# Performance work log

Hardware: AMD Instinct MI355X
Metric: run time of the kernel (lower is better)

The kernel has to match this reference:

```python
import jax, jax.numpy as jnp
import numpy as np

N_NODES = 50000
N_EDGES = 800000
IN_CH = 64
HID_CH = 128
LAT_CH = 64
N_GRAPHS = 64
U_DIM = 32


def setup_inputs() -> dict:
    key = jax.random.key(0)
    ks = jax.random.split(key, 12)
    x = jax.random.normal(ks[0], (N_NODES, IN_CH), dtype=jnp.float32)
    edge_index = jax.random.randint(ks[1], (2, N_EDGES), 0, N_NODES, dtype=jnp.int64)
    edge_attr = jax.random.normal(ks[2], (N_EDGES, 8), dtype=jnp.float32)  # unused by NodeModel
    u = jax.random.normal(ks[3], (N_GRAPHS, U_DIM), dtype=jnp.float32)
    batch = jnp.sort(jax.random.randint(ks[4], (N_NODES,), 0, N_GRAPHS, dtype=jnp.int64))
    s = 0.02
    W1 = jax.random.normal(ks[5], (2 * IN_CH, HID_CH), dtype=jnp.float32) * s
    b1 = jnp.zeros((HID_CH,), dtype=jnp.float32)
    W2 = jax.random.normal(ks[6], (HID_CH, HID_CH), dtype=jnp.float32) * s
    b2 = jnp.zeros((HID_CH,), dtype=jnp.float32)
    W3 = jax.random.normal(ks[7], (HID_CH, LAT_CH), dtype=jnp.float32) * s
    b3 = jnp.zeros((LAT_CH,), dtype=jnp.float32)
    return {"x": x, "edge_index": edge_index, "edge_attr": edge_attr, "u": u,
            "batch": batch, "W1": W1, "b1": b1, "W2": W2, "b2": b2, "W3": W3, "b3": b3}


def reference(x, edge_index, edge_attr, u, batch, W1, b1, W2, b2, W3, b3):
    row, col = edge_index[0], edge_index[1]
    # gather endpoints -> [E, 2*in_ch]
    h = jnp.concatenate([x[row], x[col]], axis=1)
    # 3-layer MLP on edges
    h = jax.nn.relu(h @ W1 + b1)
    h = jax.nn.relu(h @ W2 + b2)
    h = h @ W3 + b3  # [E, latent]
    # scatter reductions over destination node (col)
    cnt = jax.ops.segment_sum(jnp.ones((h.shape[0],), h.dtype), col, num_segments=N_NODES)
    mean = jax.ops.segment_sum(h, col, num_segments=N_NODES) / jnp.maximum(cnt, 1.0)[:, None]
    mx = jax.ops.segment_max(h, col, num_segments=N_NODES)
    mn = jax.ops.segment_min(h, col, num_segments=N_NODES)
    nonempty = (cnt > 0)[:, None]
    mx = jnp.where(nonempty, mx, 0.0)  # torch_scatter returns 0 for empty segments
    mn = jnp.where(nonempty, mn, 0.0)
    return jnp.concatenate([x, mean, mx, mn, u[batch]], axis=1)
```

## Files before the change

kernel.cpp:

```cpp
#include <hip/hip_runtime.h>

#define E_EDGES 800000
#define NN 50000
#define OUT_STRIDE 288

typedef __bf16 bf16;
typedef bf16 bf16x8 __attribute__((ext_vector_type(8)));
typedef float floatx4 __attribute__((ext_vector_type(4)));
typedef unsigned short ushort8v __attribute__((ext_vector_type(8)));

__device__ __forceinline__ unsigned short f2bf(float f){
    unsigned u = __float_as_uint(f);
    u += 0x7fffu + ((u >> 16) & 1u);
    return (unsigned short)(u >> 16);
}
__device__ __forceinline__ unsigned pack2bf(float a, float b){
    return (unsigned)f2bf(a) | ((unsigned)f2bf(b) << 16);
}
__device__ __forceinline__ unsigned encf(float f){
    unsigned u = __float_as_uint(f);
    return (u & 0x80000000u) ? ~u : (u | 0x80000000u);
}
__device__ __forceinline__ float decf(unsigned u){
    return __uint_as_float((u & 0x80000000u) ? (u ^ 0x80000000u) : ~u);
}
__device__ __forceinline__ floatx4 mfma16(ushort8v a, ushort8v b, floatx4 c){
    return __builtin_amdgcn_mfma_f32_16x16x32_bf16(
        __builtin_bit_cast(bf16x8, a), __builtin_bit_cast(bf16x8, b), c, 0, 0, 0);
}
__device__ __forceinline__ void flush_run(float* out, int node, float s, float mx, float mn, int lane){
    float* sp = out + (long)node * OUT_STRIDE + 64;
    atomicAdd(sp + lane, s);
    atomicMax((unsigned*)sp + 64 + lane, encf(mx));
    atomicMin((unsigned*)sp + 128 + lane, encf(mn));
}

#define ZC_N   12500
#define INIT_N 2400000
#define XBF_N  800000
#define PK_N   40960
#define SETUP_TOTAL (ZC_N + INIT_N + XBF_N + PK_N)

__global__ void setup_kernel(const float* __restrict__ x,
                             const float* __restrict__ W1, const float* __restrict__ W2,
                             const float* __restrict__ W3,
                             unsigned short* __restrict__ wp, unsigned short* __restrict__ xbf,
                             int* __restrict__ cnt, float* __restrict__ out)
{
    int i = blockIdx.x * blockDim.x + threadIdx.x;
    if (i < ZC_N) {
        ((int4*)cnt)[i] = make_int4(0, 0, 0, 0);
        return;
    }
    i -= ZC_N;
    if (i < INIT_N) {
        int row = i / 48, q = i % 48;
        uint4 val = (q < 32) ? make_uint4(0u, 0u, 0u, 0u)
                             : make_uint4(~0u, ~0u, ~0u, ~0u);
        ((uint4*)out)[(long)row * 72 + 16 + q] = val;
        return;
    }
    i -= INIT_N;
    if (i < XBF_N) {
        float4 v = ((const float4*)x)[i];
        ushort4 o; o.x = f2bf(v.x); o.y = f2bf(v.y); o.z = f2bf(v.z); o.w = f2bf(v.w);
        ((ushort4*)xbf)[i] = o;
        return;
    }
    i -= XBF_N;
    if (i < PK_N) {
        const float* W; int N; int idx;
        if (i < 16384)      { W = W1; N = 128; idx = i; }
        else if (i < 32768) { W = W2; N = 128; idx = i - 16384; }
        else                { W = W3; N = 64;  idx = i - 32768; }
        int j = idx & 7, lane = (idx >> 3) & 63, kc = (idx >> 9) & 3, nt = idx >> 11;
        wp[i] = f2bf(W[(kc * 32 + ((lane >> 4) & 3) * 8 + j) * N + nt * 16 + (lane & 15)]);
    }
}

__global__ void hist_kernel(const int* __restrict__ ei, int* __restrict__ cnt){
    int e = blockIdx.x * blockDim.x + threadIdx.x;
    if (e < E_EDGES) atomicAdd(&cnt[ei[E_EDGES + e]], 1);
}

__global__ void scanA_kernel(const int* __restrict__ cnt, int* __restrict__ off,
                             int* __restrict__ bsum){
    __shared__ int s[256];
    int tid = threadIdx.x;
    int node = blockIdx.x * 196 + tid;
    int val = (tid < 196 && node < NN) ? cnt[node] : 0;
    s[tid] = val;
    __syncthreads();
    for (int d = 1; d < 256; d <<= 1){
        int t = (tid >= d) ? s[tid - d] : 0;
        __syncthreads();
        s[tid] += t;
        __syncthreads();
    }
    if (tid < 196 && node < NN) off[node] = s[tid] - val;
    if (tid == 255) bsum[blockIdx.x] = s[255];
}

__global__ void scanB_kernel(const int* __restrict__ bsum, int* __restrict__ bbase){
    __shared__ int s[256];
    int tid = threadIdx.x;
    int val = bsum[tid];
    s[tid] = val;
    __syncthreads();
    for (int d = 1; d < 256; d <<= 1){
        int t = (tid >= d) ? s[tid - d] : 0;
        __syncthreads();
        s[tid] += t;
        __syncthreads();
    }
    bbase[tid] = s[tid] - val;
}

__global__ void scanC_kernel(int* __restrict__ off, const int* __restrict__ bbase){
    int n = blockIdx.x * blockDim.x + threadIdx.x;
    if (n < NN) off[n] += bbase[n / 196];
}

__global__ void scatter_kernel(const int* __restrict__ ei, int* __restrict__ off,
                               int2* __restrict__ enodes){
    int e = blockIdx.x * blockDim.x + threadIdx.x;
    if (e >= E_EDGES) return;
    int c = ei[E_EDGES + e], r = ei[e];
    int pos = atomicAdd(&off[c], 1);
    enodes[pos] = make_int2(r, c);
}

__global__ __launch_bounds__(256, 4) void edge_mlp_kernel(
    const unsigned short* __restrict__ xbf, const int2* __restrict__ enodes,
    const unsigned short* __restrict__ wp,
    const float* __restrict__ b1, const float* __restrict__ b2, const float* __restrict__ b3,
    float* __restrict__ out)
{
    __shared__ __align__(16) unsigned char smem[4 * 8704];

    const int tid  = threadIdx.x;
    const int lane = tid & 63;
    const int w    = tid >> 6;
    const int quad = lane >> 4;
    const int ln   = lane & 15;
    unsigned short* wbuf = (unsigned short*)(smem + w * 8704);
    float* Tf = (float*)wbuf;
    const ushort8v* wpv = (const ushort8v*)wp;

    const int g = blockIdx.x * 4 + w;
    const int ebase = g * 32;
    int2 ed0 = enodes[ebase + ln];
    int2 ed1 = enodes[ebase + 16 + ln];

    const ushort8v* r0 = (const ushort8v*)(xbf + (long)ed0.x * 64);
    const ushort8v* c0 = (const ushort8v*)(xbf + (long)ed0.y * 64);
    const ushort8v* r1 = (const ushort8v*)(xbf + (long)ed1.x * 64);
    const ushort8v* c1 = (const ushort8v*)(xbf + (long)ed1.y * 64);
    ushort8v B0[4] = { r0[quad], r0[4 + quad], c0[quad], c0[4 + quad] };
    ushort8v B1[4] = { r1[quad], r1[4 + quad], c1[quad], c1[4 + quad] };

#pragma unroll
    for (int nt = 0; nt < 8; nt++){
        floatx4 bini = *(const floatx4*)(b1 + nt * 16 + quad * 4);
        floatx4 a0 = bini, a1 = bini;
#pragma unroll
        for (int kc = 0; kc < 4; kc++){
            ushort8v Af = wpv[(nt * 4 + kc) * 64 + lane];
            a0 = mfma16(Af, B0[kc], a0);
            a1 = mfma16(Af, B1[kc], a1);
        }
        uint2 p0, p1;
        p0.x = pack2bf(fmaxf(a0[0], 0.f), fmaxf(a0[1], 0.f));
        p0.y = pack2bf(fmaxf(a0[2], 0.f), fmaxf(a0[3], 0.f));
        p1.x = pack2bf(fmaxf(a1[0], 0.f), fmaxf(a1[1], 0.f));
        p1.y = pack2bf(fmaxf(a1[2], 0.f), fmaxf(a1[3], 0.f));
        int col = nt * 16 + quad * 4;
        *(uint2*)(wbuf + ln * 136 + col)        = p0;
        *(uint2*)(wbuf + (16 + ln) * 136 + col) = p1;
    }

    ushort8v H0[4], H1[4];
#pragma unroll
    for (int kc = 0; kc < 4; kc++){
        H0[kc] = *(const ushort8v*)(wbuf + ln * 136 + kc * 32 + quad * 8);
        H1[kc] = *(const ushort8v*)(wbuf + (16 + ln) * 136 + kc * 32 + quad * 8);
    }
#pragma unroll
    for (int nt = 0; nt < 8; nt++){
        floatx4 bini = *(const floatx4*)(b2 + nt * 16 + quad * 4);
        floatx4 a0 = bini, a1 = bini;
#pragma unroll
        for (int kc = 0; kc < 4; kc++){
            ushort8v Af = wpv[2048 + (nt * 4 + kc) * 64 + lane];
            a0 = mfma16(Af, H0[kc], a0);
            a1 = mfma16(Af, H1[kc], a1);
        }
        uint2 p0, p1;
        p0.x = pack2bf(fmaxf(a0[0], 0.f), fmaxf(a0[1], 0.f));
        p0.y = pack2bf(fmaxf(a0[2], 0.f), fmaxf(a0[3], 0.f));
        p1.x = pack2bf(fmaxf(a1[0], 0.f), fmaxf(a1[1], 0.f));
        p1.y = pack2bf(fmaxf(a1[2], 0.f), fmaxf(a1[3], 0.f));
        int col = nt * 16 + quad * 4;
        *(uint2*)(wbuf + ln * 136 + col)        = p0;
        *(uint2*)(wbuf + (16 + ln) * 136 + col) = p1;
    }

    ushort8v G0[4], G1[4];
#pragma unroll
    for (int kc = 0; kc < 4; kc++){
        G0[kc] = *(const ushort8v*)(wbuf + ln * 136 + kc * 32 + quad * 8);
        G1[kc] = *(const ushort8v*)(wbuf + (16 + ln) * 136 + kc * 32 + quad * 8);
    }
#pragma unroll
    for (int nt = 0; nt < 4; nt++){
        floatx4 bini = *(const floatx4*)(b3 + nt * 16 + quad * 4);
        floatx4 a0 = bini, a1 = bini;
#pragma unroll
        for (int kc = 0; kc < 4; kc++){
            ushort8v Af = wpv[4096 + (nt * 4 + kc) * 64 + lane];
            a0 = mfma16(Af, G0[kc], a0);
            a1 = mfma16(Af, G1[kc], a1);
        }
        int och = nt * 16 + quad * 4;
#pragma unroll
        for (int r = 0; r < 4; r++){
            Tf[(och + r) * 33 + ln]      = a0[r];
            Tf[(och + r) * 33 + 16 + ln] = a1[r];
        }
    }

    float v[32];
#pragma unroll
    for (int j = 0; j < 32; j++) v[j] = Tf[lane * 33 + j];
    int cn0 = ed0.y, cn1 = ed1.y;
    int cur = __builtin_amdgcn_readlane(cn0, 0);
    float s = v[0], mx = v[0], mn = v[0];
#pragma unroll
    for (int j = 1; j < 32; j++){
        int nj = (j < 16) ? __builtin_amdgcn_readlane(cn0, j)
                          : __builtin_amdgcn_readlane(cn1, j - 16);
        if (nj != cur){
            flush_run(out, cur, s, mx, mn, lane);
            cur = nj; s = v[j]; mx = v[j]; mn = v[j];
        } else {
            s += v[j]; mx = fmaxf(mx, v[j]); mn = fminf(mn, v[j]);
        }
    }
    flush_run(out, cur, s, mx, mn, lane);
}

__global__ void finalize_kernel(const float* __restrict__ x, const float* __restrict__ u,
                                const int* __restrict__ batch, const int* __restrict__ cnt,
                                float* __restrict__ out)
{
    long i = (long)blockIdx.x * blockDim.x + threadIdx.x;
    if (i >= (long)NN * 72) return;
    int ndx = (int)(i / 72);
    int q   = (int)(i % 72);
    float4 res;
    if (q < 16) {
        res = ((const float4*)(x + (long)ndx * 64))[q];
    } else if (q < 32) {
        float4 sv = ((const float4*)out)[i];
        int k = cnt[ndx];
        float inv = 1.f / (float)(k > 0 ? k : 1);
        res.x = sv.x * inv; res.y = sv.y * inv; res.z = sv.z * inv; res.w = sv.w * inv;
    } else if (q < 64) {
        uint4 e = ((const uint4*)out)[i];
        bool ne = cnt[ndx] > 0;
        res.x = ne ? decf(e.x) : 0.f; res.y = ne ? decf(e.y) : 0.f;
        res.z = ne ? decf(e.z) : 0.f; res.w = ne ? decf(e.w) : 0.f;
    } else {
        res = ((const float4*)(u + (long)batch[ndx] * 32))[q - 64];
    }
    ((float4*)out)[i] = res;
}

extern "C" void kernel_launch(void* const* d_in, const int* in_sizes, int n_in,
                              void* d_out, int out_size, void* d_ws, size_t ws_size,
                              hipStream_t stream)
{
    const float* x     = (const float*)d_in[0];
    const int*   ei    = (const int*)d_in[1];
    const float* u     = (const float*)d_in[3];
    const int*   batch = (const int*)d_in[4];
    const float* W1    = (const float*)d_in[5];
    const float* b1    = (const float*)d_in[6];
    const float* W2    = (const float*)d_in[7];
    const float* b2    = (const float*)d_in[8];
    const float* W3    = (const float*)d_in[9];
    const float* b3    = (const float*)d_in[10];
    float* out = (float*)d_out;
    unsigned char* ws = (unsigned char*)d_ws;

    unsigned short* wp     = (unsigned short*)ws;
    int*            cnt    = (int*)(ws + 81920);
    int*            off    = (int*)(ws + 281920);
    int*            bsum   = (int*)(ws + 481920);
    int*            bbase  = (int*)(ws + 482944);
    int2*           enodes = (int2*)(ws + 483968);
    unsigned short* xbf    = (unsigned short*)(ws + 6883968);

    setup_kernel<<<(SETUP_TOTAL + 255) / 256, 256, 0, stream>>>(x, W1, W2, W3, wp, xbf, cnt, out);
    hist_kernel<<<(E_EDGES + 255) / 256, 256, 0, stream>>>(ei, cnt);
    scanA_kernel<<<256, 256, 0, stream>>>(cnt, off, bsum);
    scanB_kernel<<<1, 256, 0, stream>>>(bsum, bbase);
    scanC_kernel<<<(NN + 255) / 256, 256, 0, stream>>>(off, bbase);
    scatter_kernel<<<(E_EDGES + 255) / 256, 256, 0, stream>>>(ei, off, enodes);
    edge_mlp_kernel<<<6250, 256, 0, stream>>>(xbf, enodes, wp, b1, b2, b3, out);
    finalize_kernel<<<(int)(((long)NN * 72 + 255) / 256), 256, 0, stream>>>(x, u, batch, cnt, out);
}
```

Before: 327.7 us.

## Fuse histogram into setup, drop scanC, prefetch weights in MLP kernel

The histogram pass is folded into the setup kernel and the count buffer is zeroed with an async memset instead. The scanC pass is removed by adding the block base inside the scatter kernel. The edge MLP kernel now prefetches weight fragments two tiles ahead into a 3-slot register ring to hide global load latency behind the MFMAs. The bf16 conversion is switched to the compiler's native cast. The prefetch ring raises register pressure and may reduce occupancy, and the merged setup kernel runs atomics alongside streaming writes.

```diff
diff --git a/kernel.cpp b/kernel.cpp
--- a/kernel.cpp
+++ b/kernel.cpp
@@ -10,12 +10,12 @@
 typedef unsigned short ushort8v __attribute__((ext_vector_type(8)));
 
 __device__ __forceinline__ unsigned short f2bf(float f){
-    unsigned u = __float_as_uint(f);
-    u += 0x7fffu + ((u >> 16) & 1u);
-    return (unsigned short)(u >> 16);
+    return __builtin_bit_cast(unsigned short, (bf16)f);
 }
 __device__ __forceinline__ unsigned pack2bf(float a, float b){
-    return (unsigned)f2bf(a) | ((unsigned)f2bf(b) << 16);
+    unsigned short lo = __builtin_bit_cast(unsigned short, (bf16)a);
+    unsigned short hi = __builtin_bit_cast(unsigned short, (bf16)b);
+    return (unsigned)lo | ((unsigned)hi << 16);
 }
 __device__ __forceinline__ unsigned encf(float f){
     unsigned u = __float_as_uint(f);
@@ -35,24 +35,19 @@
     atomicMin((unsigned*)sp + 128 + lane, encf(mn));
 }
 
-#define ZC_N   12500
 #define INIT_N 2400000
 #define XBF_N  800000
 #define PK_N   40960
-#define SETUP_TOTAL (ZC_N + INIT_N + XBF_N + PK_N)
-
-__global__ void setup_kernel(const float* __restrict__ x,
+#define HIST_BASE (INIT_N + XBF_N + PK_N)
+#define SETUP_TOTAL (HIST_BASE + E_EDGES)
+
+__global__ void setup_kernel(const float* __restrict__ x, const int* __restrict__ ei,
                              const float* __restrict__ W1, const float* __restrict__ W2,
                              const float* __restrict__ W3,
                              unsigned short* __restrict__ wp, unsigned short* __restrict__ xbf,
                              int* __restrict__ cnt, float* __restrict__ out)
 {
     int i = blockIdx.x * blockDim.x + threadIdx.x;
-    if (i < ZC_N) {
-        ((int4*)cnt)[i] = make_int4(0, 0, 0, 0);
-        return;
-    }
-    i -= ZC_N;
     if (i < INIT_N) {
         int row = i / 48, q = i % 48;
         uint4 val = (q < 32) ? make_uint4(0u, 0u, 0u, 0u)
@@ -75,12 +70,10 @@
         else                { W = W3; N = 64;  idx = i - 32768; }
         int j = idx & 7, lane = (idx >> 3) & 63, kc = (idx >> 9) & 3, nt = idx >> 11;
         wp[i] = f2bf(W[(kc * 32 + ((lane >> 4) & 3) * 8 + j) * N + nt * 16 + (lane & 15)]);
-    }
-}
-
-__global__ void hist_kernel(const int* __restrict__ ei, int* __restrict__ cnt){
-    int e = blockIdx.x * blockDim.x + threadIdx.x;
-    if (e < E_EDGES) atomicAdd(&cnt[ei[E_EDGES + e]], 1);
+        return;
+    }
+    i -= PK_N;
+    if (i < E_EDGES) atomicAdd(&cnt[ei[E_EDGES + i]], 1);
 }
 
 __global__ void scanA_kernel(const int* __restrict__ cnt, int* __restrict__ off,
@@ -116,17 +109,12 @@
     bbase[tid] = s[tid] - val;
 }
 
-__global__ void scanC_kernel(int* __restrict__ off, const int* __restrict__ bbase){
-    int n = blockIdx.x * blockDim.x + threadIdx.x;
-    if (n < NN) off[n] += bbase[n / 196];
-}
-
 __global__ void scatter_kernel(const int* __restrict__ ei, int* __restrict__ off,
-                               int2* __restrict__ enodes){
+                               const int* __restrict__ bbase, int2* __restrict__ enodes){
     int e = blockIdx.x * blockDim.x + threadIdx.x;
     if (e >= E_EDGES) return;
     int c = ei[E_EDGES + e], r = ei[e];
-    int pos = atomicAdd(&off[c], 1);
+    int pos = atomicAdd(&off[c], 1) + bbase[c / 196];
     enodes[pos] = make_int2(r, c);
 }
 
@@ -152,6 +140,13 @@
     int2 ed0 = enodes[ebase + ln];
     int2 ed1 = enodes[ebase + 16 + ln];
 
+    ushort8v Wb[3][4];
+#define LDW(slot, idx) { _Pragma("unroll") for (int _k = 0; _k < 4; _k++) \
+        Wb[slot][_k] = wpv[(idx) * 256 + _k * 64 + lane]; }
+
+    LDW(0, 0)
+    LDW(1, 1)
+
     const ushort8v* r0 = (const ushort8v*)(xbf + (long)ed0.x * 64);
     const ushort8v* c0 = (const ushort8v*)(xbf + (long)ed0.y * 64);
     const ushort8v* r1 = (const ushort8v*)(xbf + (long)ed1.x * 64);
@@ -161,13 +156,13 @@
 
 #pragma unroll
     for (int nt = 0; nt < 8; nt++){
+        LDW((nt + 2) % 3, nt + 2)
         floatx4 bini = *(const floatx4*)(b1 + nt * 16 + quad * 4);
         floatx4 a0 = bini, a1 = bini;
 #pragma unroll
         for (int kc = 0; kc < 4; kc++){
-            ushort8v Af = wpv[(nt * 4 + kc) * 64 + lane];
-            a0 = mfma16(Af, B0[kc], a0);
-            a1 = mfma16(Af, B1[kc], a1);
+            a0 = mfma16(Wb[nt % 3][kc], B0[kc], a0);
+            a1 = mfma16(Wb[nt % 3][kc], B1[kc], a1);
         }
         uint2 p0, p1;
         p0.x = pack2bf(fmaxf(a0[0], 0.f), fmaxf(a0[1], 0.f));
@@ -187,13 +182,13 @@
     }
 #pragma unroll
     for (int nt = 0; nt < 8; nt++){
+        LDW((8 + nt + 2) % 3, 8 + nt + 2)
         floatx4 bini = *(const floatx4*)(b2 + nt * 16 + quad * 4);
         floatx4 a0 = bini, a1 = bini;
 #pragma unroll
         for (int kc = 0; kc < 4; kc++){
-            ushort8v Af = wpv[2048 + (nt * 4 + kc) * 64 + lane];
-            a0 = mfma16(Af, H0[kc], a0);
-            a1 = mfma16(Af, H1[kc], a1);
+            a0 = mfma16(Wb[(8 + nt) % 3][kc], H0[kc], a0);
+            a1 = mfma16(Wb[(8 + nt) % 3][kc], H1[kc], a1);
         }
         uint2 p0, p1;
         p0.x = pack2bf(fmaxf(a0[0], 0.f), fmaxf(a0[1], 0.f));
@@ -213,13 +208,13 @@
     }
 #pragma unroll
     for (int nt = 0; nt < 4; nt++){
+        if (nt < 2) LDW((16 + nt + 2) % 3, 16 + nt + 2)
         floatx4 bini = *(const floatx4*)(b3 + nt * 16 + quad * 4);
         floatx4 a0 = bini, a1 = bini;
 #pragma unroll
         for (int kc = 0; kc < 4; kc++){
-            ushort8v Af = wpv[4096 + (nt * 4 + kc) * 64 + lane];
-            a0 = mfma16(Af, G0[kc], a0);
-            a1 = mfma16(Af, G1[kc], a1);
+            a0 = mfma16(Wb[(16 + nt) % 3][kc], G0[kc], a0);
+            a1 = mfma16(Wb[(16 + nt) % 3][kc], G1[kc], a1);
         }
         int och = nt * 16 + quad * 4;
 #pragma unroll
@@ -301,12 +296,11 @@
     int2*           enodes = (int2*)(ws + 483968);
     unsigned short* xbf    = (unsigned short*)(ws + 6883968);
 
-    setup_kernel<<<(SETUP_TOTAL + 255) / 256, 256, 0, stream>>>(x, W1, W2, W3, wp, xbf, cnt, out);
-    hist_kernel<<<(E_EDGES + 255) / 256, 256, 0, stream>>>(ei, cnt);
+    hipMemsetAsync(cnt, 0, 200000, stream);
+    setup_kernel<<<(SETUP_TOTAL + 255) / 256, 256, 0, stream>>>(x, ei, W1, W2, W3, wp, xbf, cnt, out);
     scanA_kernel<<<256, 256, 0, stream>>>(cnt, off, bsum);
     scanB_kernel<<<1, 256, 0, stream>>>(bsum, bbase);
-    scanC_kernel<<<(NN + 255) / 256, 256, 0, stream>>>(off, bbase);
-    scatter_kernel<<<(E_EDGES + 255) / 256, 256, 0, stream>>>(ei, off, enodes);
+    scatter_kernel<<<(E_EDGES + 255) / 256, 256, 0, stream>>>(ei, off, bbase, enodes);
     edge_mlp_kernel<<<6250, 256, 0, stream>>>(xbf, enodes, wp, b1, b2, b3, out);
     finalize_kernel<<<(int)(((long)NN * 72 + 255) / 256), 256, 0, stream>>>(x, u, batch, cnt, out);
 }
```

Result: no change. 331.0 us (+1.0%).
